# Kernel optimization log

Hardware: AMD Instinct MI355X
Metric: run time of the kernel (lower is better)

## Reference

```python
import jax, jax.numpy as jnp
import numpy as np

B, NO, NM = 16, 512, 32
DO, DM, DOUT = 128, 64, 128   # in_ope_dim, in_mac_dim, out_mac_dim
H, K = 64, 16                  # external attn: num_heads*coef=8*8, k=dim//num_heads
HID = 128                      # policy hidden dim
NEG = jnp.float32(-1e30)


def _lin(x, W, b=None):
    y = x @ W.T
    return y + b if b is not None else y


def external_attention(x, W_trans, b_trans, W_l0, b_l0, W_l1, b_l1, W_proj, b_proj):
    Bx, N, C = x.shape
    x = _lin(x, W_trans, b_trans)                      # [B,N,8C]
    x = x.reshape(Bx, N, H, K).transpose(0, 2, 1, 3)   # [B,H,N,K]
    attn = _lin(x, W_l0, b_l0)
    attn = jax.nn.softmax(attn, axis=-2)               # softmax over N
    attn = attn / (1e-10 + attn.sum(-1, keepdims=True))
    x = _lin(attn, W_l1, b_l1).transpose(0, 2, 1, 3).reshape(Bx, N, H * K)
    return _lin(x, W_proj, b_proj)                     # [B,N,C]


def gat(adj, feat_ope, feat_mac, Wo, Wm, alpha_o, alpha_m):
    h_ope = feat_ope @ Wo.T                            # [B,No,D]
    h_mac = feat_mac @ Wm.T                            # [B,Nm,D]
    a_o = (h_ope * alpha_o).sum(-1)                    # [B,No]
    a_m = (h_mac * alpha_m).sum(-1)                    # [B,Nm]
    e = adj * (a_o[:, :, None] + a_m[:, None, :])      # [B,No,Nm]
    e = jnp.where(e >= 0, e, 0.2 * e)                  # leaky_relu(0.2)
    mask = adj == 1.0
    e = jnp.where(mask, e, jnp.float32(-9e10))
    alpha = jax.nn.softmax(e, axis=-2) * mask          # softmax over opes
    out_ope = jnp.einsum('bom,bod->bmd', alpha, h_ope) # [B,Nm,D]
    return out_ope + h_mac


def mlp(x, Ws, bs):
    for W, b in zip(Ws[:-1], bs[:-1]):
        x = jnp.tanh(x @ W.T + b)
    return x @ Ws[-1].T + bs[-1]


def setup_inputs() -> dict:
    key = jax.random.key(0)
    ks = jax.random.split(key, 24)
    d = {}
    d['curr_proc_adj'] = jax.random.randint(ks[0], (B, NO, NM), 0, 2).astype(jnp.float32)
    d['norm_opes'] = jax.random.normal(ks[1], (B, NO, DO), jnp.float32)
    d['norm_macs'] = jax.random.normal(ks[2], (B, NM, DM), jnp.float32)
    mask_proc = jax.random.randint(ks[3], (B, NO, NM), 0, 2).astype(bool)
    d['mask_proc'] = mask_proc
    # choose valid (unmasked) actions in the flattened [Nm, No] layout
    mask_flat = jnp.swapaxes(mask_proc, 1, 2).reshape(B, -1)
    d['action_indexes'] = jnp.argmax(mask_flat, axis=1).astype(jnp.int32)
    s = 0.05
    # external attention params (torch Linear: [out,in])
    d['W_trans'] = s * jax.random.normal(ks[4], (DO * 8, DO)); d['b_trans'] = jnp.zeros((DO * 8,))
    d['W_l0'] = s * jax.random.normal(ks[5], (K, K)); d['b_l0'] = jnp.zeros((K,))
    d['W_l1'] = s * jax.random.normal(ks[6], (K, K)); d['b_l1'] = jnp.zeros((K,))
    d['W_proj'] = s * jax.random.normal(ks[7], (DO, DO * 8)); d['b_proj'] = jnp.zeros((DO,))
    # GAT params
    d['Wo'] = s * jax.random.normal(ks[8], (DOUT, DO))
    d['Wm'] = s * jax.random.normal(ks[9], (DOUT, DM))
    d['alpha_o'] = s * jax.random.normal(ks[10], (1, 1, DOUT))
    d['alpha_m'] = s * jax.random.normal(ks[11], (1, 1, DOUT))
    # actor MLP: 512 -> 128 -> 128 -> 1
    d['A0'] = s * jax.random.normal(ks[12], (HID, 2 * DO + 2 * DOUT)); d['Ab0'] = jnp.zeros((HID,))
    d['A1'] = s * jax.random.normal(ks[13], (HID, HID)); d['Ab1'] = jnp.zeros((HID,))
    d['A2'] = s * jax.random.normal(ks[14], (1, HID)); d['Ab2'] = jnp.zeros((1,))
    # critic MLP: 256 -> 128 -> 128 -> 1
    d['C0'] = s * jax.random.normal(ks[15], (HID, DO + DOUT)); d['Cb0'] = jnp.zeros((HID,))
    d['C1'] = s * jax.random.normal(ks[16], (HID, HID)); d['Cb1'] = jnp.zeros((HID,))
    d['C2'] = s * jax.random.normal(ks[17], (1, HID)); d['Cb2'] = jnp.zeros((1,))
    return d


def reference(curr_proc_adj, norm_opes, norm_macs, mask_proc, action_indexes,
              W_trans, b_trans, W_l0, b_l0, W_l1, b_l1, W_proj, b_proj,
              Wo, Wm, alpha_o, alpha_m,
              A0, Ab0, A1, Ab1, A2, Ab2, C0, Cb0, C1, Cb1, C2, Cb2):
    h_opes = external_attention(norm_opes, W_trans, b_trans, W_l0, b_l0,
                                W_l1, b_l1, W_proj, b_proj)      # [B,No,DO]
    h_macs = gat(curr_proc_adj, norm_opes, norm_macs, Wo, Wm, alpha_o, alpha_m)  # [B,Nm,DOUT]
    h_opes_pooled = h_opes.mean(-2)   # [B,DO]
    h_macs_pooled = h_macs.mean(-2)   # [B,DOUT]
    # build h_actions directly in transposed [B, Nm, No, :] layout
    sh_o = (B, NM, NO, DO); sh_m = (B, NM, NO, DOUT)
    h_actions = jnp.concatenate([
        jnp.broadcast_to(h_opes[:, None, :, :], sh_o),
        jnp.broadcast_to(h_macs[:, :, None, :], sh_m),
        jnp.broadcast_to(h_opes_pooled[:, None, None, :], sh_o),
        jnp.broadcast_to(h_macs_pooled[:, None, None, :], sh_m)], axis=-1)
    logits = mlp(h_actions, [A0, A1, A2], [Ab0, Ab1, Ab2]).reshape(B, -1)  # [B, Nm*No]
    mask = jnp.swapaxes(mask_proc, 1, 2).reshape(B, -1)
    logits = jnp.where(mask, logits, NEG)
    logp = jax.nn.log_softmax(logits, axis=1)
    p = jnp.exp(logp)
    action_logprobs = jnp.take_along_axis(logp, action_indexes[:, None], axis=1)[:, 0]
    dist_entropys = -jnp.sum(jnp.where(mask, p * logp, 0.0), axis=1)
    h_pooled = jnp.concatenate([h_opes_pooled, h_macs_pooled], axis=-1)  # [B,256]
    state_values = mlp(h_pooled, [C0, C1, C2], [Cb0, Cb1, Cb2])[:, 0]
    return action_logprobs, state_values, dist_entropys
```

## Files before the change

### kernel.cpp

```cpp
#include <hip/hip_runtime.h>

#define BB 16
#define NO 512
#define NM 32
#define DOC 128
#define C8 1024
#define NH 64
#define KD 16

#define OFF_X12   0
#define OFF_UO    0
#define OFF_LOG   1048576
#define OFF_HOPES 8388608
#define OFF_HOPEG 9437184
#define OFF_HMAC  10485760
#define OFF_HMACS 10551296
#define OFF_AO    10616832
#define OFF_AM    10625024
#define OFF_PO    10625536
#define OFF_PM    10627584
#define OFF_UMHM  10629632
#define OFF_FLAG  10695168
#define OFF_PART  10695680
#define OFF_POPART 10700000
#define OFF_UP    10720000
#define OFF_A1P   10900000

using f32x4  = __attribute__((ext_vector_type(4))) float;
using s16x4  = __attribute__((ext_vector_type(4))) short;
using bf16x8 = __attribute__((ext_vector_type(8))) short;

__device__ __forceinline__ float fast_tanh(float x) {
  float e = __expf(2.0f * x);
  return 1.0f - 2.0f * __builtin_amdgcn_rcpf(e + 1.0f);
}

__device__ __forceinline__ short f2bf(float f) {
  unsigned u = __builtin_bit_cast(unsigned, f);
  u += 0x7FFFu + ((u >> 16) & 1u);
  return (short)(u >> 16);
}

__device__ __forceinline__ float bf2f(short s) {
  return __builtin_bit_cast(float, ((unsigned)(unsigned short)s) << 16);
}

__device__ __forceinline__ unsigned cvtpk(float a, float b) {
  unsigned r;
  asm("v_cvt_pk_bf16_f32 %0, %1, %2" : "=v"(r) : "v"(a), "v"(b));
  return r;
}

__device__ __forceinline__ bf16x8 pack8(f32x4 u0, f32x4 u1) {
  union { unsigned u[4]; bf16x8 v; } cv;
  cv.u[0] = cvtpk(u0[0], u0[1]);
  cv.u[1] = cvtpk(u0[2], u0[3]);
  cv.u[2] = cvtpk(u1[0], u1[1]);
  cv.u[3] = cvtpk(u1[2], u1[3]);
  return cv.v;
}

__device__ __forceinline__ bf16x8 pack8f(const float* t) {
  union { unsigned u[4]; bf16x8 v; } cv;
  cv.u[0] = cvtpk(t[0], t[1]);
  cv.u[1] = cvtpk(t[2], t[3]);
  cv.u[2] = cvtpk(t[4], t[5]);
  cv.u[3] = cvtpk(t[6], t[7]);
  return cv.v;
}

__device__ void probe_body(int tid, const unsigned int* __restrict__ mask,
                           int* __restrict__ flag) {
  __shared__ int s[4];
  int bad = 0;
  for (int i = tid; i < 4096; i += 256) {
    unsigned int v = mask[i];
    if (!(v == 0u || v == 1u || v == 0x3f800000u)) bad = 1;
  }
  unsigned long long any = __ballot(bad);
  int lane = tid & 63, w = tid >> 6;
  if (lane == 0) s[w] = (any != 0ull) ? 1 : 0;
  __syncthreads();
  if (tid == 0) flag[0] = s[0] | s[1] | s[2] | s[3];
}

template<int MT>
__device__ __forceinline__ void loadk(const float* xb, const float* wb,
                                      long sx, long sw, int k0,
                                      f32x4 (&xa)[MT][2], f32x4 (&wa)[4][2]) {
  #pragma unroll
  for (int mi = 0; mi < MT; ++mi) {
    xa[mi][0] = *(const f32x4*)(xb + mi * sx + k0);
    xa[mi][1] = *(const f32x4*)(xb + mi * sx + k0 + 4);
  }
  #pragma unroll
  for (int ni = 0; ni < 4; ++ni) {
    wa[ni][0] = *(const f32x4*)(wb + ni * sw + k0);
    wa[ni][1] = *(const f32x4*)(wb + ni * sw + k0 + 4);
  }
}

template<int MT>
__device__ __forceinline__ void consume(f32x4 (&xa)[MT][2], f32x4 (&wa)[4][2],
                                        f32x4 (&acc)[MT][4]) {
  bf16x8 bfr[4];
  #pragma unroll
  for (int ni = 0; ni < 4; ++ni) bfr[ni] = pack8(wa[ni][0], wa[ni][1]);
  #pragma unroll
  for (int mi = 0; mi < MT; ++mi) {
    bf16x8 af = pack8(xa[mi][0], xa[mi][1]);
    #pragma unroll
    for (int ni = 0; ni < 4; ++ni)
      acc[mi][ni] = __builtin_amdgcn_mfma_f32_16x16x32_bf16(af, bfr[ni], acc[mi][ni], 0, 0, 0);
  }
}

template<int MT>
__device__ void gemm_wave_body(int bx, int by, int tid,
    const float* __restrict__ X, const float* __restrict__ W,
    const float* __restrict__ bias, float* __restrict__ C,
    int N, int Kdim, int ldx, int ldw) {
  const int lane = tid & 63, w = tid >> 6;
  const int rowl = lane & 15, kg = lane >> 4;
  const int n0 = bx * 64;
  const int m0 = (by * 4 + w) * (MT * 16);
  const float* xb = X + (long)(m0 + rowl) * ldx + kg * 8;
  const float* wb = W + (long)(n0 + rowl) * ldw + kg * 8;
  const long sx = (long)16 * ldx, sw = (long)16 * ldw;
  f32x4 acc[MT][4] = {};
  f32x4 A0[MT][2], B0[4][2], A1[MT][2], B1[4][2];
  loadk<MT>(xb, wb, sx, sw, 0, A0, B0);
  for (int k = 0; k < Kdim; k += 64) {
    loadk<MT>(xb, wb, sx, sw, k + 32, A1, B1);
    consume<MT>(A0, B0, acc);
    if (k + 64 < Kdim) loadk<MT>(xb, wb, sx, sw, k + 64, A0, B0);
    consume<MT>(A1, B1, acc);
  }
  #pragma unroll
  for (int mi = 0; mi < MT; ++mi) {
    #pragma unroll
    for (int ni = 0; ni < 4; ++ni) {
      int col = n0 + ni * 16 + rowl;
      float bv = bias ? bias[col] : 0.0f;
      int rb = m0 + mi * 16 + kg * 4;
      #pragma unroll
      for (int r = 0; r < 4; ++r)
        C[(long)(rb + r) * N + col] = acc[mi][ni][r] + bv;
    }
  }
}

template<int MT>
__device__ void gemm_ht_body(int bx, int by, int tid,
    const float* __restrict__ X, const float* __restrict__ W,
    const float* __restrict__ bias, short* __restrict__ Ch,
    int Kdim, int ldx, int ldw) {
  const int lane = tid & 63, w = tid >> 6;
  const int rowl = lane & 15, kg = lane >> 4;
  const int n0 = bx * 64;
  const int m0 = (by * 4 + w) * (MT * 16);
  const float* xb = X + (long)(m0 + rowl) * ldx + kg * 8;
  const float* wb = W + (long)(n0 + rowl) * ldw + kg * 8;
  const long sx = (long)16 * ldx, sw = (long)16 * ldw;
  f32x4 acc[MT][4] = {};
  f32x4 A0[MT][2], B0[4][2], A1[MT][2], B1[4][2];
  loadk<MT>(xb, wb, sx, sw, 0, A0, B0);
  for (int k = 0; k < Kdim; k += 64) {
    loadk<MT>(xb, wb, sx, sw, k + 32, A1, B1);
    consume<MT>(A0, B0, acc);
    if (k + 64 < Kdim) loadk<MT>(xb, wb, sx, sw, k + 64, A0, B0);
    consume<MT>(A1, B1, acc);
  }
  #pragma unroll
  for (int mi = 0; mi < MT; ++mi) {
    #pragma unroll
    for (int ni = 0; ni < 4; ++ni) {
      int col = n0 + ni * 16 + rowl;
      float bv = bias ? bias[col] : 0.0f;
      int h = col >> 4, e = col & 15;
      int rb = m0 + mi * 16 + kg * 4;
      #pragma unroll
      for (int r = 0; r < 4; ++r) {
        int rowI = rb + r;
        int b = rowI >> 9, n = rowI & 511;
        Ch[((long)(b * 64 + h) * 512 + n) * 16 + e] = f2bf(acc[mi][ni][r] + bv);
      }
    }
  }
}

__device__ void convert_a1_body(int blk, int tid,
    const float* __restrict__ A1, short* __restrict__ A1p) {
  int i = blk * 256 + tid;
  int col = i >> 7, k = i & 127;
  A1p[((k >> 3) * 128 + col) * 8 + (k & 7)] = f2bf(A1[i]);
}

__global__ __launch_bounds__(256) void mega1_kernel(
    const float* __restrict__ nop, const float* __restrict__ Wtr,
    const float* __restrict__ btr, short* __restrict__ x12h,
    const float* __restrict__ Wo, float* __restrict__ hopeG,
    const float* __restrict__ nmac, const float* __restrict__ Wm,
    float* __restrict__ hmac,
    const float* __restrict__ A1, short* __restrict__ A1p,
    const unsigned int* __restrict__ mask, int* __restrict__ flag) {
  const int blk = blockIdx.x, tid = threadIdx.x;
  if (blk < 512) {
    gemm_ht_body<4>(blk & 15, blk >> 4, tid, nop, Wtr, btr, x12h, 128, 128, 128);
  } else if (blk < 768) {
    int t = blk - 512;
    gemm_wave_body<1>(t & 1, t >> 1, tid, nop, Wo, nullptr, hopeG, 128, 128, 128, 128);
  } else if (blk < 784) {
    int t = blk - 768;
    gemm_wave_body<1>(t & 1, t >> 1, tid, nmac, Wm, nullptr, hmac, 128, 64, 64, 64);
  } else if (blk < 848) {
    convert_a1_body(blk - 784, tid, A1, A1p);
  } else {
    probe_body(tid, mask, flag);
  }
}

__device__ void attn3_body(int b, int h, int tid, short* __restrict__ x12h,
    const float* __restrict__ W0, const float* __restrict__ b0,
    const float* __restrict__ W1, const float* __restrict__ b1) {
  __shared__ short Pb[4][128 * 16];
  __shared__ float cmw[4][16], csw[4][16];
  const int wq = tid >> 6, lane = tid & 63;
  const int rowl = lane & 15, kg = lane >> 4;
  short* slice = x12h + (long)(b * 64 + h) * 8192;
  const short* wrows = slice + (long)(wq * 128) * 16;
  const bf16x8 zero8 = {};
  bf16x8 xa[8];
  #pragma unroll
  for (int t = 0; t < 8; ++t) {
    if (kg < 2)
      xa[t] = *(const bf16x8*)(wrows + (t * 16 + rowl) * 16 + kg * 8);
    else
      xa[t] = zero8;
  }
  bf16x8 w0f = zero8;
  if (kg < 2) {
    f32x4 a = *(const f32x4*)(W0 + rowl * 16 + kg * 8);
    f32x4 c = *(const f32x4*)(W0 + rowl * 16 + kg * 8 + 4);
    w0f = pack8(a, c);
  }
  const float b0v = b0[rowl];
  f32x4 acc[8];
  #pragma unroll
  for (int t = 0; t < 8; ++t) {
    f32x4 z = {0.f, 0.f, 0.f, 0.f};
    acc[t] = __builtin_amdgcn_mfma_f32_16x16x32_bf16(xa[t], w0f, z, 0, 0, 0);
  }
  float m = -1e30f;
  #pragma unroll
  for (int t = 0; t < 8; ++t)
    #pragma unroll
    for (int r = 0; r < 4; ++r) {
      acc[t][r] += b0v;
      m = fmaxf(m, acc[t][r]);
    }
  m = fmaxf(m, __shfl_xor(m, 16));
  m = fmaxf(m, __shfl_xor(m, 32));
  if (lane < 16) cmw[wq][lane] = m;
  __syncthreads();
  const float cm = fmaxf(fmaxf(cmw[0][rowl], cmw[1][rowl]),
                         fmaxf(cmw[2][rowl], cmw[3][rowl]));
  float s = 0.f;
  #pragma unroll
  for (int t = 0; t < 8; ++t)
    #pragma unroll
    for (int r = 0; r < 4; ++r) {
      float e = __expf(acc[t][r] - cm);
      acc[t][r] = e;
      s += e;
    }
  s += __shfl_xor(s, 16);
  s += __shfl_xor(s, 32);
  if (lane < 16) csw[wq][lane] = s;
  __syncthreads();
  const float cs = csw[0][rowl] + csw[1][rowl] + csw[2][rowl] + csw[3][rowl];
  const float cinv = 1.0f / cs;
  short* pbw = Pb[wq];
  #pragma unroll
  for (int t = 0; t < 8; ++t)
    #pragma unroll
    for (int r = 0; r < 4; ++r) {
      float al = acc[t][r] * cinv;
      float rsv = al;
      rsv += __shfl_xor(rsv, 1);
      rsv += __shfl_xor(rsv, 2);
      rsv += __shfl_xor(rsv, 4);
      rsv += __shfl_xor(rsv, 8);
      float pf = al / (1e-10f + rsv);
      pbw[(t * 16 + kg * 4 + r) * 16 + rowl] = f2bf(pf);
    }
  __syncthreads();
  bf16x8 w1f = zero8;
  if (kg < 2) {
    f32x4 a = *(const f32x4*)(W1 + rowl * 16 + kg * 8);
    f32x4 c = *(const f32x4*)(W1 + rowl * 16 + kg * 8 + 4);
    w1f = pack8(a, c);
  }
  const float b1v = b1[rowl];
  #pragma unroll
  for (int t = 0; t < 8; ++t) {
    bf16x8 pa = zero8;
    if (kg < 2)
      pa = *(const bf16x8*)(pbw + (t * 16 + rowl) * 16 + kg * 8);
    f32x4 z = {0.f, 0.f, 0.f, 0.f};
    f32x4 oacc = __builtin_amdgcn_mfma_f32_16x16x32_bf16(pa, w1f, z, 0, 0, 0);
    #pragma unroll
    for (int r = 0; r < 4; ++r) {
      int n = wq * 128 + t * 16 + kg * 4 + r;
      slice[(long)n * 16 + rowl] = f2bf(oacc[r] + b1v);
    }
  }
}

__global__ __launch_bounds__(256) void mega2_kernel(
    short* __restrict__ x12h,
    const float* __restrict__ W0, const float* __restrict__ b0,
    const float* __restrict__ W1, const float* __restrict__ b1,
    const float* __restrict__ hopeG, const float* __restrict__ alo,
    float* __restrict__ ao,
    const float* __restrict__ hmac, const float* __restrict__ alm,
    float* __restrict__ am) {
  const int blk = blockIdx.x, tid = threadIdx.x;
  if (blk < 1024) {
    attn3_body(blk >> 6, blk & 63, tid, x12h, W0, b0, W1, b1);
  } else {
    int t = blk - 1024;
    int wid = t * 4 + (tid >> 6);
    int lane = tid & 63;
    const float* X; const float* al; float* out; int r;
    if (wid < 8192)       { X = hopeG; al = alo; out = ao; r = wid; }
    else if (wid < 8704)  { X = hmac;  al = alm; out = am; r = wid - 8192; }
    else return;
    const float* row = X + (long)r * 128;
    float v = fmaf(row[lane], al[lane], row[lane + 64] * al[lane + 64]);
    #pragma unroll
    for (int off = 32; off; off >>= 1) v += __shfl_down(v, off);
    if (lane == 0) out[r] = v;
  }
}

__device__ void gemm_hx_body(int bx, int by, int tid,
    const short* __restrict__ Xh, const float* __restrict__ W,
    const float* __restrict__ bias, float* __restrict__ C) {
  const int lane = tid & 63, w = tid >> 6;
  const int rowl = lane & 15, kg = lane >> 4;
  const int n0 = bx * 64;
  const int m0 = (by * 4 + w) * 16;
  const int row = m0 + rowl, b = row >> 9, n = row & 511;
  const short* xb = Xh + (long)b * 524288 + (long)n * 16 + (kg & 1) * 8;
  const long hofs = kg >> 1;
  const float* wb = W + (long)(n0 + rowl) * 1024 + kg * 8;
  const long sw = 16 * 1024L;
  f32x4 acc[4] = {};
  bf16x8 A0, A1;
  f32x4 Wb0[4][2], Wb1[4][2];
  A0 = *(const bf16x8*)(xb + hofs * 8192);
  #pragma unroll
  for (int ni = 0; ni < 4; ++ni) {
    Wb0[ni][0] = *(const f32x4*)(wb + ni * sw);
    Wb0[ni][1] = *(const f32x4*)(wb + ni * sw + 4);
  }
  for (int k = 0; k < 1024; k += 64) {
    A1 = *(const bf16x8*)(xb + (((k + 32) >> 4) + hofs) * 8192);
    #pragma unroll
    for (int ni = 0; ni < 4; ++ni) {
      Wb1[ni][0] = *(const f32x4*)(wb + ni * sw + k + 32);
      Wb1[ni][1] = *(const f32x4*)(wb + ni * sw + k + 36);
    }
    #pragma unroll
    for (int ni = 0; ni < 4; ++ni) {
      bf16x8 bfr = pack8(Wb0[ni][0], Wb0[ni][1]);
      acc[ni] = __builtin_amdgcn_mfma_f32_16x16x32_bf16(A0, bfr, acc[ni], 0, 0, 0);
    }
    if (k + 64 < 1024) {
      A0 = *(const bf16x8*)(xb + (((k + 64) >> 4) + hofs) * 8192);
      #pragma unroll
      for (int ni = 0; ni < 4; ++ni) {
        Wb0[ni][0] = *(const f32x4*)(wb + ni * sw + k + 64);
        Wb0[ni][1] = *(const f32x4*)(wb + ni * sw + k + 68);
      }
    }
    #pragma unroll
    for (int ni = 0; ni < 4; ++ni) {
      bf16x8 bfr = pack8(Wb1[ni][0], Wb1[ni][1]);
      acc[ni] = __builtin_amdgcn_mfma_f32_16x16x32_bf16(A1, bfr, acc[ni], 0, 0, 0);
    }
  }
  #pragma unroll
  for (int ni = 0; ni < 4; ++ni) {
    int col = n0 + ni * 16 + rowl;
    float bv = bias ? bias[col] : 0.0f;
    int rb = m0 + kg * 4;
    #pragma unroll
    for (int r = 0; r < 4; ++r)
      C[(long)(rb + r) * 128 + col] = acc[ni][r] + bv;
  }
}

__device__ void gat_body(int b, int m, int tid,
    const float* __restrict__ adj, const float* __restrict__ ao,
    const float* __restrict__ am, const float* __restrict__ hopeG,
    const float* __restrict__ hmac, float* __restrict__ hmacs) {
  __shared__ float al[NO];
  __shared__ float redA[4], redB[4];
  __shared__ float part[2][128];
  const int lane = tid & 63, w = tid >> 6;
  const float amv = am[b * NM + m];
  float av[2], ev[2];
  float mx = -1e30f;
  #pragma unroll
  for (int i = 0; i < 2; ++i) {
    int o = tid + i * 256;
    float a = adj[(b * NO + o) * NM + m];
    float e = ao[b * NO + o] + amv;
    e = (e >= 0.f) ? e : 0.2f * e;
    av[i] = a; ev[i] = e;
    if (a == 1.0f) mx = fmaxf(mx, e);
  }
  #pragma unroll
  for (int off = 32; off; off >>= 1) mx = fmaxf(mx, __shfl_down(mx, off));
  if (lane == 0) redA[w] = mx;
  __syncthreads();
  mx = fmaxf(fmaxf(redA[0], redA[1]), fmaxf(redA[2], redA[3]));
  float p[2], s = 0.f;
  #pragma unroll
  for (int i = 0; i < 2; ++i) {
    p[i] = (av[i] == 1.0f) ? __expf(ev[i] - mx) : 0.f;
    s += p[i];
  }
  #pragma unroll
  for (int off = 32; off; off >>= 1) s += __shfl_down(s, off);
  if (lane == 0) redB[w] = s;
  __syncthreads();
  s = redB[0] + redB[1] + redB[2] + redB[3];
  const float sinv = (s > 0.f) ? 1.0f / s : 0.f;
  al[tid] = p[0] * sinv;
  al[tid + 256] = p[1] * sinv;
  __syncthreads();
  const int d = tid & 127, og = tid >> 7;
  float acc0 = 0.f, acc1 = 0.f;
  const float* hb = hopeG + ((long)(b * NO) + og * 256) * DOC + d;
  #pragma unroll 8
  for (int i = 0; i < 256; i += 2) {
    acc0 = fmaf(al[og * 256 + i],     hb[(long)i * DOC],       acc0);
    acc1 = fmaf(al[og * 256 + i + 1], hb[(long)(i + 1) * DOC], acc1);
  }
  part[og][d] = acc0 + acc1;
  __syncthreads();
  if (og == 0)
    hmacs[(b * NM + m) * DOC + d] = part[0][d] + part[1][d]
                                   + hmac[(b * NM + m) * DOC + d];
}

__global__ __launch_bounds__(256) void mega3_kernel(
    const short* __restrict__ x12h, const float* __restrict__ Wp,
    const float* __restrict__ bp, float* __restrict__ hopes,
    const float* __restrict__ adj, const float* __restrict__ ao,
    const float* __restrict__ am, const float* __restrict__ hopeG,
    const float* __restrict__ hmac, float* __restrict__ hmacs) {
  const int blk = blockIdx.x, tid = threadIdx.x;
  if (blk < 256) {
    gemm_hx_body(blk & 1, blk >> 1, tid, x12h, Wp, bp, hopes);
  } else {
    int t = blk - 256;
    gat_body(t & 15, t >> 4, tid,
             adj, ao, am, hopeG, hmac, hmacs);
  }
}

__device__ void popart_body(int blk, int tid, const float* __restrict__ hopes,
                            float* __restrict__ popart) {
  __shared__ f32x4 part[8][32];
  const int b = blk >> 3, c = blk & 7;
  const int v4 = tid & 31, rr = tid >> 5;
  const float* base = hopes + (long)(b * 512 + c * 64 + rr * 8) * 128 + v4 * 4;
  f32x4 acc = {0.f, 0.f, 0.f, 0.f};
  #pragma unroll
  for (int i = 0; i < 8; ++i) {
    f32x4 v = *(const f32x4*)(base + (long)i * 128);
    acc[0] += v[0]; acc[1] += v[1]; acc[2] += v[2]; acc[3] += v[3];
  }
  part[rr][v4] = acc;
  __syncthreads();
  if (rr == 0) {
    f32x4 s = part[0][v4];
    #pragma unroll
    for (int i = 1; i < 8; ++i) {
      f32x4 t = part[i][v4];
      s[0] += t[0]; s[1] += t[1]; s[2] += t[2]; s[3] += t[3];
    }
    *(f32x4*)(popart + (long)blk * 128 + v4 * 4) = s;
  }
}

__device__ void pmpool_body(int b, int tid, const float* __restrict__ hmacs,
                            float* __restrict__ pm) {
  __shared__ f32x4 part[8][32];
  const int v4 = tid & 31, rr = tid >> 5;
  const float* base = hmacs + (long)(b * 32 + rr * 4) * 128 + v4 * 4;
  f32x4 acc = {0.f, 0.f, 0.f, 0.f};
  #pragma unroll
  for (int i = 0; i < 4; ++i) {
    f32x4 v = *(const f32x4*)(base + (long)i * 128);
    acc[0] += v[0]; acc[1] += v[1]; acc[2] += v[2]; acc[3] += v[3];
  }
  part[rr][v4] = acc;
  __syncthreads();
  if (rr == 0) {
    f32x4 s = part[0][v4];
    #pragma unroll
    for (int i = 1; i < 8; ++i) {
      f32x4 t = part[i][v4];
      s[0] += t[0]; s[1] += t[1]; s[2] += t[2]; s[3] += t[3];
    }
    const float inv = 1.0f / 32.0f;
    s[0] *= inv; s[1] *= inv; s[2] *= inv; s[3] *= inv;
    *(f32x4*)(pm + (long)b * 128 + v4 * 4) = s;
  }
}

__global__ __launch_bounds__(256) void mega4_kernel(
    const float* __restrict__ hopes, const float* __restrict__ hmacs,
    float* __restrict__ popart, float* __restrict__ pm,
    const float* __restrict__ A0, float* __restrict__ Uo,
    float* __restrict__ umhm) {
  const int blk = blockIdx.x, tid = threadIdx.x;
  if (blk < 128) {
    popart_body(blk, tid, hopes, popart);
  } else if (blk < 144) {
    pmpool_body(blk - 128, tid, hmacs, pm);
  } else if (blk < 400) {
    int t = blk - 144;
    gemm_wave_body<1>(t & 1, t >> 1, tid, hopes, A0, nullptr, Uo, 128, 128, 128, 512);
  } else {
    int t = blk - 400;
    gemm_wave_body<1>(t & 1, t >> 1, tid, hmacs, A0 + 128, nullptr, umhm, 128, 128, 128, 512);
  }
}

__global__ __launch_bounds__(128) void mega5_kernel(
    const float* __restrict__ popart, float* __restrict__ po,
    const float* __restrict__ pm, const float* __restrict__ A0,
    const float* __restrict__ Ab0, float* __restrict__ up) {
  __shared__ float pos[128], pms[128];
  const int b = blockIdx.x, j = threadIdx.x;
  float s = 0.f;
  #pragma unroll
  for (int c = 0; c < 8; ++c) s += popart[(b * 8 + c) * 128 + j];
  s *= (1.0f / 512.0f);
  po[b * 128 + j] = s;
  pos[j] = s;
  pms[j] = pm[b * 128 + j];
  __syncthreads();
  const float* a1 = A0 + (long)j * 512 + 256;
  const float* a2 = A0 + (long)j * 512 + 384;
  float acc = Ab0[j];
  #pragma unroll 4
  for (int k4 = 0; k4 < 32; ++k4) {
    f32x4 av = *(const f32x4*)(a1 + k4 * 4);
    acc = fmaf(av[0], pos[k4 * 4], acc);
    acc = fmaf(av[1], pos[k4 * 4 + 1], acc);
    acc = fmaf(av[2], pos[k4 * 4 + 2], acc);
    acc = fmaf(av[3], pos[k4 * 4 + 3], acc);
  }
  #pragma unroll 4
  for (int k4 = 0; k4 < 32; ++k4) {
    f32x4 av = *(const f32x4*)(a2 + k4 * 4);
    acc = fmaf(av[0], pms[k4 * 4], acc);
    acc = fmaf(av[1], pms[k4 * 4 + 1], acc);
    acc = fmaf(av[2], pms[k4 * 4 + 2], acc);
    acc = fmaf(av[3], pms[k4 * 4 + 3], acc);
  }
  up[b * 128 + j] = acc;
}

__global__ __launch_bounds__(256) void actor_mfma8_kernel(
    const float* __restrict__ Uo, const float* __restrict__ umhm,
    const float* __restrict__ up, const short* __restrict__ A1p,
    const float* __restrict__ Ab1, const float* __restrict__ A2,
    const float* __restrict__ Ab2, float* __restrict__ logits) {
  const int tid = threadIdx.x;
  const int blk = blockIdx.x;
  const int oc = blk & 7;
  const int mg = (blk >> 3) & 7;
  const int b  = blk >> 6;
  const int obase = oc * 64;
  const int m0 = mg * 4;
  const int lane = tid & 63, w = tid >> 6;
  const int rowl = lane & 15, kg = lane >> 4;
  const float* uo = Uo + (long)(b * NO + obase + w * 16 + rowl) * 128;
  const float* upb = up + b * 128;
  const float* umb = umhm + (b * NM + m0) * 128;
  bf16x8 af[4][4];
  #pragma unroll
  for (int kk = 0; kk < 4; ++kk) {
    int kb = kk * 32 + kg * 8;
    f32x4 u0 = *(const f32x4*)(uo + kb);
    f32x4 u1 = *(const f32x4*)(uo + kb + 4);
    f32x4 p0 = *(const f32x4*)(upb + kb);
    f32x4 p1 = *(const f32x4*)(upb + kb + 4);
    float base0[4], base1[4];
    #pragma unroll
    for (int e = 0; e < 4; ++e) {
      base0[e] = u0[e] + p0[e];
      base1[e] = u1[e] + p1[e];
    }
    #pragma unroll
    for (int mi = 0; mi < 4; ++mi) {
      f32x4 a0 = *(const f32x4*)(umb + mi * 128 + kb);
      f32x4 a1 = *(const f32x4*)(umb + mi * 128 + kb + 4);
      float t[8];
      #pragma unroll
      for (int e = 0; e < 4; ++e) {
        t[e]     = fast_tanh(base0[e] + a0[e]);
        t[4 + e] = fast_tanh(base1[e] + a1[e]);
      }
      af[mi][kk] = pack8f(t);
    }
  }
  float pr[4][4] = {};
  #pragma unroll
  for (int ct = 0; ct < 8; ++ct) {
    const int col = ct * 16 + rowl;
    bf16x8 bf[4];
    #pragma unroll
    for (int kk = 0; kk < 4; ++kk)
      bf[kk] = *(const bf16x8*)(A1p + ((kk * 4 + kg) * 128 + col) * 8);
    f32x4 ac[4] = {};
    #pragma unroll
    for (int kk = 0; kk < 4; ++kk)
      #pragma unroll
      for (int mi = 0; mi < 4; ++mi)
        ac[mi] = __builtin_amdgcn_mfma_f32_16x16x32_bf16(af[mi][kk], bf[kk], ac[mi], 0, 0, 0);
    const float ab = Ab1[col], a2c = A2[col];
    #pragma unroll
    for (int mi = 0; mi < 4; ++mi)
      #pragma unroll
      for (int r = 0; r < 4; ++r) {
        float z = fast_tanh(ac[mi][r] + ab);
        pr[mi][r] = fmaf(a2c, z, pr[mi][r]);
      }
  }
  const float ab2 = Ab2[0];
  const long base0 = ((long)b << 14) + (long)m0 * 512 + obase + w * 16 + kg * 4;
  #pragma unroll
  for (int r = 0; r < 4; ++r) {
    float v0 = pr[0][r], v1 = pr[1][r], v2 = pr[2][r], v3 = pr[3][r];
    #pragma unroll
    for (int off = 1; off < 16; off <<= 1) {
      v0 += __shfl_xor(v0, off);
      v1 += __shfl_xor(v1, off);
      v2 += __shfl_xor(v2, off);
      v3 += __shfl_xor(v3, off);
    }
    if (rowl == 0) {
      logits[base0 + r] = v0 + ab2;
      logits[base0 + 512 + r] = v1 + ab2;
      logits[base0 + 1024 + r] = v2 + ab2;
      logits[base0 + 1536 + r] = v3 + ab2;
    }
  }
}

__global__ __launch_bounds__(1024) void final_part1(
    const float* __restrict__ logits, const void* __restrict__ maskp,
    const int* __restrict__ flag, float* __restrict__ part) {
  __shared__ float sm[16];
  const int b = blockIdx.x, c = blockIdx.y;
  const int tid = threadIdx.x;
  const int lane = tid & 63, w = tid >> 6;
  const bool word_mode = (flag[0] == 0);
  const unsigned int* mw = (const unsigned int*)maskp;
  const unsigned char* mb = (const unsigned char*)maskp;
  const int i = c * 1024 + tid;
  const int o = i & 511, mm = i >> 9;
  const int mofs = (b * NO + o) * NM + mm;
  const bool msk = word_mode ? (mw[mofs] != 0u) : (mb[mofs] != 0);
  const float x = logits[b * (NM * NO) + i];
  float mx = msk ? x : -1e30f;
  #pragma unroll
  for (int off = 32; off; off >>= 1) mx = fmaxf(mx, __shfl_down(mx, off));
  if (lane == 0) sm[w] = mx;
  __syncthreads();
  if (tid == 0) {
    float m2 = sm[0];
    #pragma unroll
    for (int k = 1; k < 16; ++k) m2 = fmaxf(m2, sm[k]);
    sm[0] = m2;
  }
  __syncthreads();
  const float M = sm[0];
  float S = 0.f, T = 0.f;
  if (msk) {
    float d = x - M;
    float e = __expf(d);
    S = e; T = e * d;
  }
  #pragma unroll
  for (int off = 32; off; off >>= 1) { S += __shfl_down(S, off); T += __shfl_down(T, off); }
  __syncthreads();
  __shared__ float ss[16], st[16];
  if (lane == 0) { ss[w] = S; st[w] = T; }
  __syncthreads();
  if (tid == 0) {
    float St = 0.f, Tt = 0.f;
    #pragma unroll
    for (int k = 0; k < 16; ++k) { St += ss[k]; Tt += st[k]; }
    float* pp = part + (b * 16 + c) * 3;
    pp[0] = M; pp[1] = St; pp[2] = Tt;
  }
}

__global__ __launch_bounds__(128) void final2c_kernel(
    const float* __restrict__ part, const float* __restrict__ logits,
    const int* __restrict__ aidx,
    const float* __restrict__ po, const float* __restrict__ pm,
    const float* __restrict__ C0, const float* __restrict__ Cb0,
    const float* __restrict__ C1, const float* __restrict__ Cb1,
    const float* __restrict__ C2, const float* __restrict__ Cb2,
    float* __restrict__ out) {
  if (blockIdx.x < 16) {
    if (threadIdx.x >= 64) return;
    const int b = blockIdx.x;
    const int lane = threadIdx.x;
    float lm = -3e30f, lS = 0.f, lT = 0.f;
    if (lane < 16) {
      const float* pp = part + (b * 16 + lane) * 3;
      lm = pp[0]; lS = pp[1]; lT = pp[2];
    }
    float M = lm;
    #pragma unroll
    for (int off = 8; off; off >>= 1) M = fmaxf(M, __shfl_xor(M, off, 16));
    float wgt = (lane < 16) ? __expf(lm - M) : 0.f;
    float S = wgt * lS;
    float T = wgt * (lT + (lm - M) * lS);
    #pragma unroll
    for (int off = 8; off; off >>= 1) {
      S += __shfl_xor(S, off, 16);
      T += __shfl_xor(T, off, 16);
    }
    if (lane == 0) {
      float lSm = logf(S);
      out[b] = logits[b * (NM * NO) + aidx[b]] - M - lSm;
      out[32 + b] = lSm - T / S;
    }
  } else {
    __shared__ float v[256];
    __shared__ float z[128];
    __shared__ float sc[2];
    const int b = blockIdx.x - 16;
    const int j = threadIdx.x;
    v[j] = po[b * 128 + j];
    v[128 + j] = pm[b * 128 + j];
    __syncthreads();
    float acc = Cb0[j];
    for (int k = 0; k < 256; ++k) acc = fmaf(C0[j * 256 + k], v[k], acc);
    z[j] = fast_tanh(acc);
    __syncthreads();
    acc = Cb1[j];
    for (int k = 0; k < 128; ++k) acc = fmaf(C1[j * 128 + k], z[k], acc);
    float z2 = fast_tanh(acc);
    float p = C2[j] * z2;
    #pragma unroll
    for (int off = 32; off; off >>= 1) p += __shfl_down(p, off);
    const int lane = j & 63, w = j >> 6;
    if (lane == 0) sc[w] = p;
    __syncthreads();
    if (j == 0) out[16 + b] = sc[0] + sc[1] + Cb2[0];
  }
}

extern "C" void kernel_launch(void* const* d_in, const int* in_sizes, int n_in,
                              void* d_out, int out_size, void* d_ws, size_t ws_size,
                              hipStream_t stream) {
  (void)in_sizes; (void)n_in; (void)out_size; (void)ws_size;
  const float* adj  = (const float*)d_in[0];
  const float* nop  = (const float*)d_in[1];
  const float* nmac = (const float*)d_in[2];
  const void*  maskp = d_in[3];
  const int*   aidx = (const int*)d_in[4];
  const float* Wtr  = (const float*)d_in[5];
  const float* btr  = (const float*)d_in[6];
  const float* W0   = (const float*)d_in[7];
  const float* b0   = (const float*)d_in[8];
  const float* W1   = (const float*)d_in[9];
  const float* b1   = (const float*)d_in[10];
  const float* Wp   = (const float*)d_in[11];
  const float* bp   = (const float*)d_in[12];
  const float* Wo   = (const float*)d_in[13];
  const float* Wm   = (const float*)d_in[14];
  const float* alo  = (const float*)d_in[15];
  const float* alm  = (const float*)d_in[16];
  const float* A0   = (const float*)d_in[17];
  const float* Ab0  = (const float*)d_in[18];
  const float* A1   = (const float*)d_in[19];
  const float* Ab1  = (const float*)d_in[20];
  const float* A2   = (const float*)d_in[21];
  const float* Ab2  = (const float*)d_in[22];
  const float* C0   = (const float*)d_in[23];
  const float* Cb0  = (const float*)d_in[24];
  const float* C1   = (const float*)d_in[25];
  const float* Cb1  = (const float*)d_in[26];
  const float* C2   = (const float*)d_in[27];
  const float* Cb2  = (const float*)d_in[28];

  float* ws     = (float*)d_ws;
  short* x12h   = (short*)(ws + OFF_X12);
  float* hopes  = ws + OFF_HOPES;
  float* hopeG  = ws + OFF_HOPEG;
  float* hmac   = ws + OFF_HMAC;
  float* hmacs  = ws + OFF_HMACS;
  float* ao     = ws + OFF_AO;
  float* am     = ws + OFF_AM;
  float* po     = ws + OFF_PO;
  float* pm     = ws + OFF_PM;
  float* Uo     = ws + OFF_UO;
  float* umhm   = ws + OFF_UMHM;
  float* logits = ws + OFF_LOG;
  float* popart = ws + OFF_POPART;
  float* up     = ws + OFF_UP;
  short* A1p    = (short*)(ws + OFF_A1P);
  int*   flag   = (int*)(ws + OFF_FLAG);
  float* partb  = ws + OFF_PART;
  float* outp   = (float*)d_out;

  mega1_kernel<<<849, 256, 0, stream>>>(nop, Wtr, btr, x12h, Wo, hopeG,
                                        nmac, Wm, hmac, A1, A1p,
                                        (const unsigned int*)maskp, flag);
  mega2_kernel<<<3200, 256, 0, stream>>>(x12h, W0, b0, W1, b1,
                                         hopeG, alo, ao, hmac, alm, am);
  mega3_kernel<<<768, 256, 0, stream>>>(x12h, Wp, bp, hopes,
                                        adj, ao, am, hopeG, hmac, hmacs);
  mega4_kernel<<<416, 256, 0, stream>>>(hopes, hmacs, popart, pm, A0, Uo, umhm);
  mega5_kernel<<<16, 128, 0, stream>>>(popart, po, pm, A0, Ab0, up);
  actor_mfma8_kernel<<<1024, 256, 0, stream>>>(Uo, umhm, up, A1p, Ab1, A2, Ab2, logits);
  final_part1<<<dim3(16, 16), 1024, 0, stream>>>(logits, maskp, flag, partb);
  final2c_kernel<<<32, 128, 0, stream>>>(partb, logits, aidx,
                                         po, pm, C0, Cb0, C1, Cb1, C2, Cb2, outp);
}
```

Baseline: 144.7 us.

## Fuse masked softmax partial reduction into actor MFMA kernel epilogue

The actor kernel now loads the action mask itself after computing its logits. It computes per-wave online-softmax partials (max, sum of exp, sum of exp times offset), merges them across lanes with a log-sum-exp merge helper, and writes one triple per wave. This removes the separate final_part1 launch and its re-read of the full logits buffer. The final kernel now merges 256 partials per batch instead of 16. In exchange, the actor epilogue does extra strided mask loads and exp work.

```diff
diff --git a/kernel.cpp b/kernel.cpp
--- a/kernel.cpp
+++ b/kernel.cpp
@@ -21,9 +21,9 @@
 #define OFF_PM    10627584
 #define OFF_UMHM  10629632
 #define OFF_FLAG  10695168
-#define OFF_PART  10695680
 #define OFF_POPART 10700000
 #define OFF_UP    10720000
+#define OFF_PART2 10750000
 #define OFF_A1P   10900000
 
 using f32x4  = __attribute__((ext_vector_type(4))) float;
@@ -67,6 +67,15 @@
   cv.u[2] = cvtpk(t[4], t[5]);
   cv.u[3] = cvtpk(t[6], t[7]);
   return cv.v;
+}
+
+__device__ __forceinline__ void smmerge(float& lm, float& lS, float& lT,
+                                        float om, float oS, float oT) {
+  float nm = fmaxf(lm, om);
+  float ea = __expf(lm - nm), eb = __expf(om - nm);
+  lT = (lT + (lm - nm) * lS) * ea + (oT + (om - nm) * oS) * eb;
+  lS = lS * ea + oS * eb;
+  lm = nm;
 }
 
 __device__ void probe_body(int tid, const unsigned int* __restrict__ mask,
@@ -579,11 +588,13 @@
   up[b * 128 + j] = acc;
 }
 
-__global__ __launch_bounds__(256) void actor_mfma8_kernel(
+__global__ __launch_bounds__(256) void actor_mfma9_kernel(
     const float* __restrict__ Uo, const float* __restrict__ umhm,
     const float* __restrict__ up, const short* __restrict__ A1p,
     const float* __restrict__ Ab1, const float* __restrict__ A2,
-    const float* __restrict__ Ab2, float* __restrict__ logits) {
+    const float* __restrict__ Ab2, const void* __restrict__ maskp,
+    const int* __restrict__ flag, float* __restrict__ logits,
+    float* __restrict__ partw) {
   const int tid = threadIdx.x;
   const int blk = blockIdx.x;
   const int oc = blk & 7;
@@ -647,7 +658,7 @@
       }
   }
   const float ab2 = Ab2[0];
-  const long base0 = ((long)b << 14) + (long)m0 * 512 + obase + w * 16 + kg * 4;
+  float rv[4][4];
   #pragma unroll
   for (int r = 0; r < 4; ++r) {
     float v0 = pr[0][r], v1 = pr[1][r], v2 = pr[2][r], v3 = pr[3][r];
@@ -658,61 +669,65 @@
       v2 += __shfl_xor(v2, off);
       v3 += __shfl_xor(v3, off);
     }
-    if (rowl == 0) {
-      logits[base0 + r] = v0 + ab2;
-      logits[base0 + 512 + r] = v1 + ab2;
-      logits[base0 + 1024 + r] = v2 + ab2;
-      logits[base0 + 1536 + r] = v3 + ab2;
-    }
-  }
-}
-
-__global__ __launch_bounds__(1024) void final_part1(
-    const float* __restrict__ logits, const void* __restrict__ maskp,
-    const int* __restrict__ flag, float* __restrict__ part) {
-  __shared__ float sm[16];
-  const int b = blockIdx.x, c = blockIdx.y;
-  const int tid = threadIdx.x;
-  const int lane = tid & 63, w = tid >> 6;
+    rv[r][0] = v0 + ab2; rv[r][1] = v1 + ab2;
+    rv[r][2] = v2 + ab2; rv[r][3] = v3 + ab2;
+  }
+  const long base0 = ((long)b << 14) + (long)m0 * 512 + obase + w * 16 + kg * 4;
+  if (rowl == 0) {
+    #pragma unroll
+    for (int r = 0; r < 4; ++r) {
+      logits[base0 + r]        = rv[r][0];
+      logits[base0 + 512 + r]  = rv[r][1];
+      logits[base0 + 1024 + r] = rv[r][2];
+      logits[base0 + 1536 + r] = rv[r][3];
+    }
+  }
   const bool word_mode = (flag[0] == 0);
-  const unsigned int* mw = (const unsigned int*)maskp;
-  const unsigned char* mb = (const unsigned char*)maskp;
-  const int i = c * 1024 + tid;
-  const int o = i & 511, mm = i >> 9;
-  const int mofs = (b * NO + o) * NM + mm;
-  const bool msk = word_mode ? (mw[mofs] != 0u) : (mb[mofs] != 0);
-  const float x = logits[b * (NM * NO) + i];
-  float mx = msk ? x : -1e30f;
-  #pragma unroll
-  for (int off = 32; off; off >>= 1) mx = fmaxf(mx, __shfl_down(mx, off));
-  if (lane == 0) sm[w] = mx;
-  __syncthreads();
-  if (tid == 0) {
-    float m2 = sm[0];
-    #pragma unroll
-    for (int k = 1; k < 16; ++k) m2 = fmaxf(m2, sm[k]);
-    sm[0] = m2;
-  }
-  __syncthreads();
-  const float M = sm[0];
-  float S = 0.f, T = 0.f;
-  if (msk) {
-    float d = x - M;
-    float e = __expf(d);
-    S = e; T = e * d;
-  }
-  #pragma unroll
-  for (int off = 32; off; off >>= 1) { S += __shfl_down(S, off); T += __shfl_down(T, off); }
-  __syncthreads();
-  __shared__ float ss[16], st[16];
-  if (lane == 0) { ss[w] = S; st[w] = T; }
-  __syncthreads();
-  if (tid == 0) {
-    float St = 0.f, Tt = 0.f;
-    #pragma unroll
-    for (int k = 0; k < 16; ++k) { St += ss[k]; Tt += st[k]; }
-    float* pp = part + (b * 16 + c) * 3;
-    pp[0] = M; pp[1] = St; pp[2] = Tt;
+  const int ob = obase + w * 16 + kg * 4;
+  bool mk[4][4];
+  if (word_mode) {
+    const unsigned int* mw = (const unsigned int*)maskp;
+    #pragma unroll
+    for (int r = 0; r < 4; ++r) {
+      long mo = (long)(b * NO + ob + r) * NM + m0;
+      #pragma unroll
+      for (int mi = 0; mi < 4; ++mi) mk[r][mi] = (mw[mo + mi] != 0u);
+    }
+  } else {
+    const unsigned char* mb = (const unsigned char*)maskp;
+    #pragma unroll
+    for (int r = 0; r < 4; ++r) {
+      long mo = (long)(b * NO + ob + r) * NM + m0;
+      #pragma unroll
+      for (int mi = 0; mi < 4; ++mi) mk[r][mi] = (mb[mo + mi] != 0);
+    }
+  }
+  float lm = -1e30f;
+  #pragma unroll
+  for (int r = 0; r < 4; ++r)
+    #pragma unroll
+    for (int mi = 0; mi < 4; ++mi)
+      if (mk[r][mi]) lm = fmaxf(lm, rv[r][mi]);
+  float lS = 0.f, lT = 0.f;
+  #pragma unroll
+  for (int r = 0; r < 4; ++r)
+    #pragma unroll
+    for (int mi = 0; mi < 4; ++mi)
+      if (mk[r][mi]) {
+        float d = rv[r][mi] - lm;
+        float e = __expf(d);
+        lS += e; lT += e * d;
+      }
+  #pragma unroll
+  for (int off = 16; off < 64; off <<= 1) {
+    float om = __shfl_xor(lm, off);
+    float oS = __shfl_xor(lS, off);
+    float oT = __shfl_xor(lT, off);
+    smmerge(lm, lS, lT, om, oS, oT);
+  }
+  if (lane == 0) {
+    float* pp = partw + ((long)blk * 4 + w) * 3;
+    pp[0] = lm; pp[1] = lS; pp[2] = lT;
   }
 }
 
@@ -729,25 +744,21 @@
     const int b = blockIdx.x;
     const int lane = threadIdx.x;
     float lm = -3e30f, lS = 0.f, lT = 0.f;
-    if (lane < 16) {
-      const float* pp = part + (b * 16 + lane) * 3;
-      lm = pp[0]; lS = pp[1]; lT = pp[2];
-    }
-    float M = lm;
-    #pragma unroll
-    for (int off = 8; off; off >>= 1) M = fmaxf(M, __shfl_xor(M, off, 16));
-    float wgt = (lane < 16) ? __expf(lm - M) : 0.f;
-    float S = wgt * lS;
-    float T = wgt * (lT + (lm - M) * lS);
-    #pragma unroll
-    for (int off = 8; off; off >>= 1) {
-      S += __shfl_xor(S, off, 16);
-      T += __shfl_xor(T, off, 16);
+    const float* pp = part + ((long)b * 256 + lane * 4) * 3;
+    #pragma unroll
+    for (int t = 0; t < 4; ++t)
+      smmerge(lm, lS, lT, pp[t * 3], pp[t * 3 + 1], pp[t * 3 + 2]);
+    #pragma unroll
+    for (int off = 1; off < 64; off <<= 1) {
+      float om = __shfl_xor(lm, off);
+      float oS = __shfl_xor(lS, off);
+      float oT = __shfl_xor(lT, off);
+      smmerge(lm, lS, lT, om, oS, oT);
     }
     if (lane == 0) {
-      float lSm = logf(S);
-      out[b] = logits[b * (NM * NO) + aidx[b]] - M - lSm;
-      out[32 + b] = lSm - T / S;
+      float lSm = logf(lS);
+      out[b] = logits[b * (NM * NO) + aidx[b]] - lm - lSm;
+      out[32 + b] = lSm - lT / lS;
     }
   } else {
     __shared__ float v[256];
@@ -826,7 +837,7 @@
   float* up     = ws + OFF_UP;
   short* A1p    = (short*)(ws + OFF_A1P);
   int*   flag   = (int*)(ws + OFF_FLAG);
-  float* partb  = ws + OFF_PART;
+  float* partw  = ws + OFF_PART2;
   float* outp   = (float*)d_out;
 
   mega1_kernel<<<849, 256, 0, stream>>>(nop, Wtr, btr, x12h, Wo, hopeG,
@@ -838,8 +849,8 @@
                                         adj, ao, am, hopeG, hmac, hmacs);
   mega4_kernel<<<416, 256, 0, stream>>>(hopes, hmacs, popart, pm, A0, Uo, umhm);
   mega5_kernel<<<16, 128, 0, stream>>>(popart, po, pm, A0, Ab0, up);
-  actor_mfma8_kernel<<<1024, 256, 0, stream>>>(Uo, umhm, up, A1p, Ab1, A2, Ab2, logits);
-  final_part1<<<dim3(16, 16), 1024, 0, stream>>>(logits, maskp, flag, partb);
-  final2c_kernel<<<32, 128, 0, stream>>>(partb, logits, aidx,
+  actor_mfma9_kernel<<<1024, 256, 0, stream>>>(Uo, umhm, up, A1p, Ab1, A2, Ab2,
+                                               maskp, flag, logits, partw);
+  final2c_kernel<<<32, 128, 0, stream>>>(partw, logits, aidx,
                                          po, pm, C0, Cb0, C1, Cb1, C2, Cb2, outp);
 }
```

Measured after the change: 141.0 us. -2.6%, faster.
